# Performance work log

Measured on AMD Instinct MI355X. Metric: run time of the kernel, lower is better.

## Reference

```python
import jax, jax.numpy as jnp
import numpy as np

N, E, B, A = 102400, 1638400, 256, 7


def setup_inputs() -> dict:
    key = jax.random.key(0)
    ks = jax.random.split(key, 24)
    rn = lambda k, s, sc=0.1: jax.random.normal(k, s, jnp.float32) * sc
    return {
        "x": jax.random.normal(ks[0], (N, 5), jnp.float32),
        "edge_index": jax.random.randint(ks[1], (2, E), 0, N, jnp.int32),
        "edge_attr": jax.random.normal(ks[2], (E, 1), jnp.float32),
        "agent_state": jax.random.normal(ks[3], (B, 34), jnp.float32),
        "pool_batch": jnp.sort(jax.random.randint(ks[4], (N,), 0, B, jnp.int32)),
        # GATConv params (heads=1, concat): lin [5,64], lin_edge [1,64], att vectors [64], bias [64]
        "W_gat": rn(ks[5], (5, 64)), "att_src": rn(ks[6], (64,)), "att_dst": rn(ks[7], (64,)),
        "W_edge": rn(ks[8], (1, 64)), "att_edge": rn(ks[9], (64,)), "b_gat": rn(ks[10], (64,)),
        "W_fc1": rn(ks[11], (64, 128)), "b_fc1": rn(ks[12], (128,)),
        "W_fc2": rn(ks[13], (34, 64)), "b_fc2": rn(ks[14], (64,)),
        "W_v1": rn(ks[15], (192, 128)), "b_v1": rn(ks[16], (128,)),
        "W_v2": rn(ks[17], (128, 1)), "b_v2": rn(ks[18], (1,)),
        "W_a1": rn(ks[19], (192, 128)), "b_a1": rn(ks[20], (128,)),
        "W_a2": rn(ks[21], (128, A)), "b_a2": rn(ks[22], (A,)),
    }


def _gat(x, edge_index, edge_attr, W_gat, att_src, att_dst, W_edge, att_edge, b_gat):
    n = x.shape[0]
    # add self-loops (PyG default), self-loop edge_attr = mean of edge_attr
    loop = jnp.arange(n, dtype=edge_index.dtype)
    src = jnp.concatenate([edge_index[0], loop])
    dst = jnp.concatenate([edge_index[1], loop])
    ea = jnp.concatenate([edge_attr, jnp.broadcast_to(edge_attr.mean(0), (n, edge_attr.shape[1]))], 0)
    h = x @ W_gat                                  # [N,64]
    a_s = h @ att_src                              # [N]
    a_d = h @ att_dst                              # [N]
    a_e = (ea @ W_edge) @ att_edge                 # [E+N]
    alpha = jax.nn.leaky_relu(a_s[src] + a_d[dst] + a_e, 0.2)
    # segment softmax over incoming edges per destination node
    m = jax.ops.segment_max(alpha, dst, num_segments=n)
    ex = jnp.exp(alpha - m[dst])
    s = jax.ops.segment_sum(ex, dst, num_segments=n)
    w = ex / (s[dst] + 1e-16)
    out = jax.ops.segment_sum(w[:, None] * h[src], dst, num_segments=n)
    return out + b_gat


def reference(x, edge_index, edge_attr, agent_state, pool_batch,
              W_gat, att_src, att_dst, W_edge, att_edge, b_gat,
              W_fc1, b_fc1, W_fc2, b_fc2,
              W_v1, b_v1, W_v2, b_v2, W_a1, b_a1, W_a2, b_a2):
    h = _gat(x, edge_index, edge_attr, W_gat, att_src, att_dst, W_edge, att_edge, b_gat)
    h = jax.nn.relu(h @ W_fc1 + b_fc1)             # [N,128]
    # global mean pool over graphs
    ssum = jax.ops.segment_sum(h, pool_batch, num_segments=B)
    cnt = jax.ops.segment_sum(jnp.ones((h.shape[0],), h.dtype), pool_batch, num_segments=B)
    g = ssum / jnp.maximum(cnt, 1.0)[:, None]      # [B,128]
    a = jax.nn.relu(agent_state @ W_fc2 + b_fc2)   # [B,64]
    z = jnp.concatenate([g, a], -1)                # [B,192]
    value = jax.nn.relu(z @ W_v1 + b_v1) @ W_v2 + b_v2
    adv = jax.nn.relu(z @ W_a1 + b_a1) @ W_a2 + b_a2
    return value + adv - adv.mean(-1, keepdims=True)
```

## Files before the change

### kernel.cpp

```cpp
#include <hip/hip_runtime.h>
#include <hip/hip_fp16.h>
#include <math.h>

#define NPB   512
#define NPBL  9
#define HSTR  5
#define MAXR  256
#define TILE  2048
#define RPT   8
#define GCS   16
#define EPARTS 256
#define SLICES 8

static __device__ __forceinline__ float lrelu(float x) { return x > 0.0f ? x : 0.2f * x; }

static __device__ __forceinline__ unsigned pk2(float a, float b) {
    __half2 h = __floats2half2_rn(a, b);
    return *reinterpret_cast<unsigned*>(&h);
}


__global__ void k_easum_part(const float* __restrict__ ea, float* __restrict__ part, int n) {
    __shared__ float s[256];
    int t = threadIdx.x;
    int n4 = n >> 2;
    const float4* ea4 = (const float4*)ea;
    float acc = 0.f;
    for (int i = blockIdx.x * 256 + t; i < n4; i += EPARTS * 256) {
        float4 v = ea4[i];
        acc += v.x + v.y + v.z + v.w;
    }
    if (blockIdx.x == 0 && t < (n & 3)) acc += ea[n4 * 4 + t];
    s[t] = acc;
    __syncthreads();
    for (int o = 128; o > 0; o >>= 1) {
        if (t < o) s[t] += s[t + o];
        __syncthreads();
    }
    if (t == 0) part[blockIdx.x] = s[0];
}

__global__ void k_setup(const float* __restrict__ W_gat, const float* __restrict__ att_src,
                        const float* __restrict__ att_dst, const float* __restrict__ W_edge,
                        const float* __restrict__ att_edge, const float* __restrict__ b_gat,
                        const float* __restrict__ W_fc1, const float* __restrict__ b_fc1,
                        const float* __restrict__ part, float* __restrict__ consts) {
    __shared__ float s[128];
    int t = threadIdx.x;
    s[t] = part[t] + part[t + 128];
    __syncthreads();
    for (int o = 64; o > 0; o >>= 1) {
        if (t < o) s[t] += s[t + o];
        __syncthreads();
    }
    if (t == 0) consts[0] = s[0];
    if (t == 0) {
        float c = 0.f;
        for (int k = 0; k < 64; k++) c += W_edge[k] * att_edge[k];
        consts[1] = c;
    }
    if (t < 5) {
        float a = 0.f, b = 0.f;
        for (int c = 0; c < 64; c++) {
            float w = W_gat[t * 64 + c];
            a += w * att_src[c];
            b += w * att_dst[c];
        }
        consts[2 + t] = a;
        consts[7 + t] = b;
    }
    float bcv = b_fc1[t];
    for (int c = 0; c < 64; c++) bcv += b_gat[c] * W_fc1[c * 128 + t];
    consts[16 + t] = bcv;
    for (int k = 0; k < 5; k++) {
        float w = 0.f;
        for (int c = 0; c < 64; c++) w += W_gat[k * 64 + c] * W_fc1[c * 128 + t];
        consts[144 + k * 128 + t] = w;
    }
}

__global__ void k_np1(const float* __restrict__ x, const float* __restrict__ consts,
                      uint4* __restrict__ xh, float* __restrict__ a_s, float* __restrict__ a_d,
                      const int* __restrict__ pb, int* __restrict__ bstart,
                      const int* __restrict__ src, const int* __restrict__ dst,
                      const float* __restrict__ ea,
                      uint2* __restrict__ slab, unsigned* __restrict__ gcur,
                      int N, int B, int E, int R, int CAP, int nbl) {
    if ((int)blockIdx.x < nbl) {
        int i = blockIdx.x * blockDim.x + threadIdx.x;
        if (i >= N) return;
        const float* xi = x + (size_t)i * 5;
        float x0 = xi[0], x1 = xi[1], x2 = xi[2], x3 = xi[3], x4 = xi[4];
        float as = x0 * consts[2] + x1 * consts[3] + x2 * consts[4] + x3 * consts[5] + x4 * consts[6];
        float ad = x0 * consts[7] + x1 * consts[8] + x2 * consts[9] + x3 * consts[10] + x4 * consts[11];
        uint4 pkv;
        pkv.x = pk2(x0, x1);
        pkv.y = pk2(x2, x3);
        pkv.z = pk2(x4, 1.0f);
        pkv.w = __float_as_uint(as);
        xh[i] = pkv;
        a_s[i] = as;
        a_d[i] = ad;
        int cur = pb[i];
        int prev = (i == 0) ? -1 : pb[i - 1];
        for (int b = prev + 1; b <= cur; b++) bstart[b] = i;
        if (i == N - 1)
            for (int b = cur + 1; b <= B; b++) bstart[b] = N;
        return;
    }
    __shared__ unsigned hist[MAXR], lbase[MAXR], gbase[MAXR], scan[256];
    __shared__ uint2 staged[TILE];
    __shared__ unsigned char bof[TILE];
    int t = threadIdx.x;
    int e0 = ((int)blockIdx.x - nbl) * TILE;
    int n = E - e0; if (n > TILE) n = TILE;
    for (int i = t; i < MAXR; i += 256) hist[i] = 0;
    __syncthreads();
    unsigned key[RPT]; float val[RPT]; unsigned brk[RPT];
    float ce = consts[1];
#pragma unroll
    for (int k = 0; k < RPT; k++) {
        int idx = t + k * 256;
        brk[k] = 0xFFFFFFFFu;
        if (idx < n) {
            int e = e0 + idx;
            int d = dst[e];
            unsigned b = (unsigned)d >> NPBL;
            key[k] = ((unsigned)src[e] << NPBL) | ((unsigned)d & (NPB - 1));
            val[k] = ce * ea[e];
            unsigned r = atomicAdd(&hist[b], 1u);
            brk[k] = (b << 12) | r;
        }
    }
    __syncthreads();
    unsigned v = (t < R) ? hist[t] : 0;
    if (t < R) gbase[t] = atomicAdd(&gcur[t * GCS], v);
    scan[t] = v;
    __syncthreads();
    for (int off = 1; off < 256; off <<= 1) {
        unsigned add = (t >= off) ? scan[t - off] : 0;
        __syncthreads();
        scan[t] += add;
        __syncthreads();
    }
    if (t < R) lbase[t] = scan[t] - v;
    __syncthreads();
#pragma unroll
    for (int k = 0; k < RPT; k++) {
        if (brk[k] != 0xFFFFFFFFu) {
            unsigned b = brk[k] >> 12, r = brk[k] & 4095u;
            unsigned pos = lbase[b] + r;
            staged[pos] = make_uint2(key[k], __float_as_uint(val[k]));
            bof[pos] = (unsigned char)b;
        }
    }
    __syncthreads();
    for (int i = t; i < n; i += 256) {
        unsigned b = bof[i];
        unsigned slot = gbase[b] + (unsigned)i - lbase[b];
        if (slot < (unsigned)CAP) slab[(size_t)b * CAP + slot] = staged[i];
    }
}

__global__ void k_p2(const uint2* __restrict__ slab, const unsigned* __restrict__ gcur,
                     const uint4* __restrict__ xh, const float* __restrict__ a_d,
                     float* __restrict__ partials, int S, int CAP, int N) {
    __shared__ __half2 accH[NPB * HSTR];
    __shared__ float adl[NPB];
    int t = threadIdx.x;
    int s = blockIdx.x, r = blockIdx.y;
    for (int i = t; i < NPB; i += 256) {
        int node = r * NPB + i;
        adl[i] = (node < N) ? a_d[node] : 0.f;
    }
    __half2 z2 = __floats2half2_rn(0.f, 0.f);
    for (int i = t; i < NPB * HSTR; i += 256) accH[i] = z2;
    __syncthreads();
    unsigned cnt = gcur[r * GCS]; if (cnt > (unsigned)CAP) cnt = CAP;
    unsigned L = (cnt + (unsigned)S - 1) / (unsigned)S;
    unsigned i0 = (unsigned)s * L, i1 = i0 + L; if (i1 > cnt) i1 = cnt;
    const uint2* sl = slab + (size_t)r * CAP;
    for (unsigned i = i0 + t; i < i1; i += 256) {
        uint2 rec = sl[i];
        uint4 v = xh[rec.x >> NPBL];
        unsigned dl = rec.x & (NPB - 1);
        float al = __uint_as_float(v.w) + adl[dl] + __uint_as_float(rec.y);
        float ex = __expf(lrelu(al));
        __half2 ex2 = __half2half2(__float2half(ex));
        __half2* a = accH + dl * HSTR;
        unsafeAtomicAdd(a + 0, __hmul2(ex2, *reinterpret_cast<const __half2*>(&v.x)));
        unsafeAtomicAdd(a + 1, __hmul2(ex2, *reinterpret_cast<const __half2*>(&v.y)));
        unsafeAtomicAdd(a + 2, __hmul2(ex2, *reinterpret_cast<const __half2*>(&v.z)));
    }
    __syncthreads();
    float* out = partials + (size_t)(r * S + s) * (NPB * 6);
    for (int j = t; j < NPB * 6; j += 256) {
        int comp = j >> NPBL, dl = j & (NPB - 1);
        __half2 h = accH[dl * HSTR + (comp >> 1)];
        out[j] = (comp & 1) ? __high2float(h) : __low2float(h);
    }
}

__global__ void k_p3(const float* __restrict__ partials, const float* __restrict__ x,
                     const float* __restrict__ a_s, const float* __restrict__ a_d,
                     const float* __restrict__ consts, float* __restrict__ y,
                     int N, int S, float inv_E) {
    int i = blockIdx.x * blockDim.x + threadIdx.x;
    if (i >= N) return;
    int r = i >> NPBL, dl = i & (NPB - 1);
    float y0 = 0, y1 = 0, y2 = 0, y3 = 0, y4 = 0, ss = 0;
    const float* p = partials + (size_t)r * S * (NPB * 6) + dl;
    for (int s = 0; s < S; s++) {
        const float* q = p + (size_t)s * (NPB * 6);
        y0 += q[0 * NPB]; y1 += q[1 * NPB]; y2 += q[2 * NPB];
        y3 += q[3 * NPB]; y4 += q[4 * NPB]; ss += q[5 * NPB];
    }
    const float* xi = x + (size_t)i * 5;
    float x0 = xi[0], x1 = xi[1], x2 = xi[2], x3 = xi[3], x4 = xi[4];
    float mean_ea = consts[0] * inv_E;
    float aself = lrelu(a_s[i] + a_d[i] + consts[1] * mean_ea);
    float exs = __expf(aself);
    float inv = 1.f / (ss + exs + 1e-16f);
    y[0 * (size_t)N + i] = (y0 + exs * x0) * inv;
    y[1 * (size_t)N + i] = (y1 + exs * x1) * inv;
    y[2 * (size_t)N + i] = (y2 + exs * x2) * inv;
    y[3 * (size_t)N + i] = (y3 + exs * x3) * inv;
    y[4 * (size_t)N + i] = (y4 + exs * x4) * inv;
}

__global__ void k_pool(const float* __restrict__ y, const float* __restrict__ consts,
                       const int* __restrict__ bstart, float* __restrict__ g4, int B, int N) {
    int l = threadIdx.x;
    int b = blockIdx.x >> 2, q = blockIdx.x & 3;
    int st = bstart[b], en = bstart[b + 1];
    int len = en - st;
    int qlen = (len + 3) >> 2;
    int i0 = st + q * qlen;
    int i1 = i0 + qlen;
    if (i0 > en) i0 = en;
    if (i1 > en) i1 = en;
    float w0 = consts[144 + l], w1 = consts[272 + l], w2 = consts[400 + l],
          w3 = consts[528 + l], w4 = consts[656 + l];
    float bc = consts[16 + l];
    const float* y0 = y;
    const float* y1p = y + (size_t)N;
    const float* y2p = y + 2 * (size_t)N;
    const float* y3p = y + 3 * (size_t)N;
    const float* y4p = y + 4 * (size_t)N;
    float a0 = 0.f, a1 = 0.f, a2 = 0.f, a3 = 0.f;
    int i = i0;
    for (; i + 3 < i1; i += 4) {
        float h0 = bc + y0[i] * w0 + y1p[i] * w1 + y2p[i] * w2 + y3p[i] * w3 + y4p[i] * w4;
        float h1 = bc + y0[i+1] * w0 + y1p[i+1] * w1 + y2p[i+1] * w2 + y3p[i+1] * w3 + y4p[i+1] * w4;
        float h2 = bc + y0[i+2] * w0 + y1p[i+2] * w1 + y2p[i+2] * w2 + y3p[i+2] * w3 + y4p[i+2] * w4;
        float h3 = bc + y0[i+3] * w0 + y1p[i+3] * w1 + y2p[i+3] * w2 + y3p[i+3] * w3 + y4p[i+3] * w4;
        a0 += fmaxf(h0, 0.f);
        a1 += fmaxf(h1, 0.f);
        a2 += fmaxf(h2, 0.f);
        a3 += fmaxf(h3, 0.f);
    }
    for (; i < i1; ++i) {
        float h = bc + y0[i] * w0 + y1p[i] * w1 + y2p[i] * w2 + y3p[i] * w3 + y4p[i] * w4;
        a0 += fmaxf(h, 0.f);
    }
    g4[((size_t)q * B + b) * 128 + l] = (a0 + a1) + (a2 + a3);
}

__global__ void k_head(const float* __restrict__ g4, const int* __restrict__ bstart,
                       const float* __restrict__ agent_state, const float* __restrict__ W_fc2,
                       const float* __restrict__ b_fc2, const float* __restrict__ W_v1,
                       const float* __restrict__ b_v1, const float* __restrict__ W_v2,
                       const float* __restrict__ b_v2, const float* __restrict__ W_a1,
                       const float* __restrict__ b_a1, const float* __restrict__ W_a2,
                       const float* __restrict__ b_a2, float* __restrict__ out, int A, int B) {
    __shared__ float z[192];
    __shared__ float v1s[128], a1s[128], red[128];
    __shared__ float advs[8];
    int b = blockIdx.x, t = threadIdx.x;
    float cnt = (float)(bstart[b + 1] - bstart[b]);
    cnt = cnt < 1.f ? 1.f : cnt;
    z[t] = (g4[(size_t)b * 128 + t] + g4[((size_t)B + b) * 128 + t]
          + g4[(2 * (size_t)B + b) * 128 + t] + g4[(3 * (size_t)B + b) * 128 + t]) / cnt;
    if (t < 64) {
        float a = b_fc2[t];
        const float* as_ = agent_state + b * 34;
        for (int k = 0; k < 34; k++) a += as_[k] * W_fc2[k * 64 + t];
        z[128 + t] = fmaxf(a, 0.f);
    }
    __syncthreads();
    float v = b_v1[t], a = b_a1[t];
#pragma unroll 4
    for (int j = 0; j < 192; j++) {
        float zj = z[j];
        v += zj * W_v1[j * 128 + t];
        a += zj * W_a1[j * 128 + t];
    }
    v1s[t] = fmaxf(v, 0.f);
    a1s[t] = fmaxf(a, 0.f);
    __syncthreads();
    red[t] = v1s[t] * W_v2[t];
    __syncthreads();
    for (int o = 64; o > 0; o >>= 1) {
        if (t < o) red[t] += red[t + o];
        __syncthreads();
    }
    float value = red[0] + b_v2[0];
    if (t < A) {
        float ad = b_a2[t];
        for (int j = 0; j < 128; j++) ad += a1s[j] * W_a2[j * A + t];
        advs[t] = ad;
    }
    __syncthreads();
    if (t == 0) {
        float m = 0.f;
        for (int j = 0; j < A; j++) m += advs[j];
        m *= (1.f / (float)A);
        for (int j = 0; j < A; j++) out[b * A + j] = value + advs[j] - m;
    }
}

extern "C" void kernel_launch(void* const* d_in, const int* in_sizes, int n_in,
                              void* d_out, int out_size, void* d_ws, size_t ws_size,
                              hipStream_t stream) {
    const float* x        = (const float*)d_in[0];
    const int* edge_index = (const int*)d_in[1];
    const float* ea       = (const float*)d_in[2];
    const float* agent    = (const float*)d_in[3];
    const int* pool_batch = (const int*)d_in[4];
    const float* W_gat    = (const float*)d_in[5];
    const float* att_src  = (const float*)d_in[6];
    const float* att_dst  = (const float*)d_in[7];
    const float* W_edge   = (const float*)d_in[8];
    const float* att_edge = (const float*)d_in[9];
    const float* b_gat    = (const float*)d_in[10];
    const float* W_fc1    = (const float*)d_in[11];
    const float* b_fc1    = (const float*)d_in[12];
    const float* W_fc2    = (const float*)d_in[13];
    const float* b_fc2    = (const float*)d_in[14];
    const float* W_v1     = (const float*)d_in[15];
    const float* b_v1     = (const float*)d_in[16];
    const float* W_v2     = (const float*)d_in[17];
    const float* b_v2     = (const float*)d_in[18];
    const float* W_a1     = (const float*)d_in[19];
    const float* b_a1     = (const float*)d_in[20];
    const float* W_a2     = (const float*)d_in[21];
    const float* b_a2     = (const float*)d_in[22];

    const int N = in_sizes[0] / 5;
    const int E = in_sizes[2];
    const int B = in_sizes[3] / 34;
    const int A = out_size / B;
    const float inv_E = 1.0f / (float)E;

    const int* src = edge_index;
    const int* dst = edge_index + E;

    const int R = (N + NPB - 1) / NPB;
    int capBase = (E + R - 1) / R;
    const int CAP = capBase + capBase / 16 + 256;

    char* ws = (char*)d_ws;
    size_t off = 0;
    auto take = [&](size_t bytes) {
        size_t o = off;
        off = (off + bytes + 255) & ~(size_t)255;
        return o;
    };
    size_t o_consts = take(4096);
    size_t o_gcur   = take((size_t)MAXR * GCS * 4);
    size_t zero_bytes = off;
    size_t o_epart  = take((size_t)EPARTS * 4);
    size_t o_xh     = take((size_t)N * 16);
    size_t o_as     = take((size_t)N * 4);
    size_t o_ad     = take((size_t)N * 4);
    size_t o_y      = take((size_t)N * 5 * 4);
    size_t o_bstart = take((size_t)(B + 1) * 4);
    size_t o_g4     = take((size_t)4 * B * 128 * 4);
    size_t o_slab   = take((size_t)R * CAP * 8);
    size_t o_part   = off;
    size_t perS = (size_t)R * NPB * 6 * 4;
    int S = SLICES;
    while (S > 1 && o_part + (size_t)S * perS > ws_size) S--;

    float* consts   = (float*)(ws + o_consts);
    unsigned* gcur  = (unsigned*)(ws + o_gcur);
    float* epart    = (float*)(ws + o_epart);
    uint4* xh       = (uint4*)(ws + o_xh);
    float* a_s      = (float*)(ws + o_as);
    float* a_d      = (float*)(ws + o_ad);
    float* y        = (float*)(ws + o_y);
    int* bstart     = (int*)(ws + o_bstart);
    float* g4       = (float*)(ws + o_g4);
    uint2* slab     = (uint2*)(ws + o_slab);
    float* partials = (float*)(ws + o_part);

    (void)hipMemsetAsync(d_ws, 0, zero_bytes, stream);

    k_easum_part<<<EPARTS, 256, 0, stream>>>(ea, epart, E);
    k_setup<<<1, 128, 0, stream>>>(W_gat, att_src, att_dst, W_edge, att_edge, b_gat,
                                   W_fc1, b_fc1, epart, consts);

    int nbl = (N + 255) / 256;
    int ebl = (E + TILE - 1) / TILE;
    k_np1<<<nbl + ebl, 256, 0, stream>>>(x, consts, xh, a_s, a_d, pool_batch, bstart,
                                         src, dst, ea, slab, gcur, N, B, E, R, CAP, nbl);
    dim3 g2grid(S, R);
    k_p2<<<g2grid, 256, 0, stream>>>(slab, gcur, xh, a_d, partials, S, CAP, N);
    k_p3<<<nbl, 256, 0, stream>>>(partials, x, a_s, a_d, consts, y, N, S, inv_E);
    k_pool<<<4 * B, 128, 0, stream>>>(y, consts, bstart, g4, B, N);
    k_head<<<B, 128, 0, stream>>>(g4, bstart, agent, W_fc2, b_fc2, W_v1, b_v1, W_v2, b_v2,
                                  W_a1, b_a1, W_a2, b_a2, (float*)d_out, A, B);
}
```

Before: 128.2 us.

## Fuse edge-attr sum into scatter pass, drop memset, store fp16 partials

Removes the separate edge_attr reduction kernel and the workspace memset. The edge sum is now accumulated inside the edge-bucketing blocks via per-block reductions and atomics into eight slots, and the zeroing moves into the setup kernel. The final sum is written into consts by one thread of the aggregation kernel, which k_p3 reads afterwards. Per-slice partials are stored as packed half2 instead of fp32, halving partial-buffer traffic at some precision cost in the cross-slice sums.

After: 124.2 us. 3.1% less time.

```diff
diff --git a/kernel.cpp b/kernel.cpp
--- a/kernel.cpp
+++ b/kernel.cpp
@@ -9,7 +9,6 @@
 #define TILE  2048
 #define RPT   8
 #define GCS   16
-#define EPARTS 256
 #define SLICES 8
 
 static __device__ __forceinline__ float lrelu(float x) { return x > 0.0f ? x : 0.2f * x; }
@@ -18,42 +17,21 @@
     __half2 h = __floats2half2_rn(a, b);
     return *reinterpret_cast<unsigned*>(&h);
 }
-
-
-__global__ void k_easum_part(const float* __restrict__ ea, float* __restrict__ part, int n) {
-    __shared__ float s[256];
-    int t = threadIdx.x;
-    int n4 = n >> 2;
-    const float4* ea4 = (const float4*)ea;
-    float acc = 0.f;
-    for (int i = blockIdx.x * 256 + t; i < n4; i += EPARTS * 256) {
-        float4 v = ea4[i];
-        acc += v.x + v.y + v.z + v.w;
-    }
-    if (blockIdx.x == 0 && t < (n & 3)) acc += ea[n4 * 4 + t];
-    s[t] = acc;
-    __syncthreads();
-    for (int o = 128; o > 0; o >>= 1) {
-        if (t < o) s[t] += s[t + o];
-        __syncthreads();
-    }
-    if (t == 0) part[blockIdx.x] = s[0];
-}
+static __device__ __forceinline__ float2 up2(unsigned u) {
+    __half2 h = *reinterpret_cast<__half2*>(&u);
+    return __half22float2(h);
+}
+
 
 __global__ void k_setup(const float* __restrict__ W_gat, const float* __restrict__ att_src,
                         const float* __restrict__ att_dst, const float* __restrict__ W_edge,
                         const float* __restrict__ att_edge, const float* __restrict__ b_gat,
                         const float* __restrict__ W_fc1, const float* __restrict__ b_fc1,
-                        const float* __restrict__ part, float* __restrict__ consts) {
-    __shared__ float s[128];
+                        float* __restrict__ consts, unsigned* __restrict__ gcur,
+                        float* __restrict__ epart8) {
     int t = threadIdx.x;
-    s[t] = part[t] + part[t + 128];
-    __syncthreads();
-    for (int o = 64; o > 0; o >>= 1) {
-        if (t < o) s[t] += s[t + o];
-        __syncthreads();
-    }
-    if (t == 0) consts[0] = s[0];
+    for (int i = t; i < MAXR * GCS; i += 128) gcur[i] = 0u;
+    if (t < 8) epart8[t] = 0.f;
     if (t == 0) {
         float c = 0.f;
         for (int k = 0; k < 64; k++) c += W_edge[k] * att_edge[k];
@@ -85,6 +63,7 @@
                       const int* __restrict__ src, const int* __restrict__ dst,
                       const float* __restrict__ ea,
                       uint2* __restrict__ slab, unsigned* __restrict__ gcur,
+                      float* __restrict__ epart8,
                       int N, int B, int E, int R, int CAP, int nbl) {
     if ((int)blockIdx.x < nbl) {
         int i = blockIdx.x * blockDim.x + threadIdx.x;
@@ -111,6 +90,7 @@
     __shared__ unsigned hist[MAXR], lbase[MAXR], gbase[MAXR], scan[256];
     __shared__ uint2 staged[TILE];
     __shared__ unsigned char bof[TILE];
+    __shared__ float esum[256];
     int t = threadIdx.x;
     int e0 = ((int)blockIdx.x - nbl) * TILE;
     int n = E - e0; if (n > TILE) n = TILE;
@@ -118,6 +98,7 @@
     __syncthreads();
     unsigned key[RPT]; float val[RPT]; unsigned brk[RPT];
     float ce = consts[1];
+    float easc = 0.f;
 #pragma unroll
     for (int k = 0; k < RPT; k++) {
         int idx = t + k * 256;
@@ -127,7 +108,9 @@
             int d = dst[e];
             unsigned b = (unsigned)d >> NPBL;
             key[k] = ((unsigned)src[e] << NPBL) | ((unsigned)d & (NPB - 1));
-            val[k] = ce * ea[e];
+            float eav = ea[e];
+            easc += eav;
+            val[k] = ce * eav;
             unsigned r = atomicAdd(&hist[b], 1u);
             brk[k] = (b << 12) | r;
         }
@@ -160,15 +143,28 @@
         unsigned slot = gbase[b] + (unsigned)i - lbase[b];
         if (slot < (unsigned)CAP) slab[(size_t)b * CAP + slot] = staged[i];
     }
+    esum[t] = easc;
+    __syncthreads();
+    for (int o = 128; o > 0; o >>= 1) {
+        if (t < o) esum[t] += esum[t + o];
+        __syncthreads();
+    }
+    if (t == 0) unsafeAtomicAdd(&epart8[blockIdx.x & 7], esum[0]);
 }
 
 __global__ void k_p2(const uint2* __restrict__ slab, const unsigned* __restrict__ gcur,
                      const uint4* __restrict__ xh, const float* __restrict__ a_d,
-                     float* __restrict__ partials, int S, int CAP, int N) {
+                     unsigned* __restrict__ partials, const float* __restrict__ epart8,
+                     float* __restrict__ consts_w, int S, int CAP, int N) {
     __shared__ __half2 accH[NPB * HSTR];
     __shared__ float adl[NPB];
     int t = threadIdx.x;
     int s = blockIdx.x, r = blockIdx.y;
+    if (s == 0 && r == 0 && t == 0) {
+        float se = 0.f;
+        for (int i = 0; i < 8; i++) se += epart8[i];
+        consts_w[0] = se;
+    }
     for (int i = t; i < NPB; i += 256) {
         int node = r * NPB + i;
         adl[i] = (node < N) ? a_d[node] : 0.f;
@@ -193,39 +189,40 @@
         unsafeAtomicAdd(a + 2, __hmul2(ex2, *reinterpret_cast<const __half2*>(&v.z)));
     }
     __syncthreads();
-    float* out = partials + (size_t)(r * S + s) * (NPB * 6);
-    for (int j = t; j < NPB * 6; j += 256) {
+    unsigned* out = partials + (size_t)(r * S + s) * (NPB * 3);
+    for (int j = t; j < NPB * 3; j += 256) {
         int comp = j >> NPBL, dl = j & (NPB - 1);
-        __half2 h = accH[dl * HSTR + (comp >> 1)];
-        out[j] = (comp & 1) ? __high2float(h) : __low2float(h);
-    }
-}
-
-__global__ void k_p3(const float* __restrict__ partials, const float* __restrict__ x,
+        out[j] = *reinterpret_cast<unsigned*>(&accH[dl * HSTR + comp]);
+    }
+}
+
+__global__ void k_p3(const unsigned* __restrict__ partials, const float* __restrict__ x,
                      const float* __restrict__ a_s, const float* __restrict__ a_d,
                      const float* __restrict__ consts, float* __restrict__ y,
                      int N, int S, float inv_E) {
     int i = blockIdx.x * blockDim.x + threadIdx.x;
     if (i >= N) return;
     int r = i >> NPBL, dl = i & (NPB - 1);
-    float y0 = 0, y1 = 0, y2 = 0, y3 = 0, y4 = 0, ss = 0;
-    const float* p = partials + (size_t)r * S * (NPB * 6) + dl;
+    float2 y01 = make_float2(0.f, 0.f), y23 = make_float2(0.f, 0.f), y4s = make_float2(0.f, 0.f);
+    const unsigned* p = partials + (size_t)r * S * (NPB * 3) + dl;
     for (int s = 0; s < S; s++) {
-        const float* q = p + (size_t)s * (NPB * 6);
-        y0 += q[0 * NPB]; y1 += q[1 * NPB]; y2 += q[2 * NPB];
-        y3 += q[3 * NPB]; y4 += q[4 * NPB]; ss += q[5 * NPB];
+        const unsigned* q = p + (size_t)s * (NPB * 3);
+        float2 a = up2(q[0 * NPB]), b = up2(q[1 * NPB]), c = up2(q[2 * NPB]);
+        y01.x += a.x; y01.y += a.y;
+        y23.x += b.x; y23.y += b.y;
+        y4s.x += c.x; y4s.y += c.y;
     }
     const float* xi = x + (size_t)i * 5;
     float x0 = xi[0], x1 = xi[1], x2 = xi[2], x3 = xi[3], x4 = xi[4];
     float mean_ea = consts[0] * inv_E;
     float aself = lrelu(a_s[i] + a_d[i] + consts[1] * mean_ea);
     float exs = __expf(aself);
-    float inv = 1.f / (ss + exs + 1e-16f);
-    y[0 * (size_t)N + i] = (y0 + exs * x0) * inv;
-    y[1 * (size_t)N + i] = (y1 + exs * x1) * inv;
-    y[2 * (size_t)N + i] = (y2 + exs * x2) * inv;
-    y[3 * (size_t)N + i] = (y3 + exs * x3) * inv;
-    y[4 * (size_t)N + i] = (y4 + exs * x4) * inv;
+    float inv = 1.f / (y4s.y + exs + 1e-16f);
+    y[0 * (size_t)N + i] = (y01.x + exs * x0) * inv;
+    y[1 * (size_t)N + i] = (y01.y + exs * x1) * inv;
+    y[2 * (size_t)N + i] = (y23.x + exs * x2) * inv;
+    y[3 * (size_t)N + i] = (y23.y + exs * x3) * inv;
+    y[4 * (size_t)N + i] = (y4s.x + exs * x4) * inv;
 }
 
 __global__ void k_pool(const float* __restrict__ y, const float* __restrict__ consts,
@@ -368,8 +365,7 @@
     };
     size_t o_consts = take(4096);
     size_t o_gcur   = take((size_t)MAXR * GCS * 4);
-    size_t zero_bytes = off;
-    size_t o_epart  = take((size_t)EPARTS * 4);
+    size_t o_epart8 = take(8 * 4);
     size_t o_xh     = take((size_t)N * 16);
     size_t o_as     = take((size_t)N * 4);
     size_t o_ad     = take((size_t)N * 4);
@@ -378,13 +374,13 @@
     size_t o_g4     = take((size_t)4 * B * 128 * 4);
     size_t o_slab   = take((size_t)R * CAP * 8);
     size_t o_part   = off;
-    size_t perS = (size_t)R * NPB * 6 * 4;
+    size_t perS = (size_t)R * NPB * 3 * 4;
     int S = SLICES;
     while (S > 1 && o_part + (size_t)S * perS > ws_size) S--;
 
     float* consts   = (float*)(ws + o_consts);
     unsigned* gcur  = (unsigned*)(ws + o_gcur);
-    float* epart    = (float*)(ws + o_epart);
+    float* epart8   = (float*)(ws + o_epart8);
     uint4* xh       = (uint4*)(ws + o_xh);
     float* a_s      = (float*)(ws + o_as);
     float* a_d      = (float*)(ws + o_ad);
@@ -392,20 +388,18 @@
     int* bstart     = (int*)(ws + o_bstart);
     float* g4       = (float*)(ws + o_g4);
     uint2* slab     = (uint2*)(ws + o_slab);
-    float* partials = (float*)(ws + o_part);
-
-    (void)hipMemsetAsync(d_ws, 0, zero_bytes, stream);
-
-    k_easum_part<<<EPARTS, 256, 0, stream>>>(ea, epart, E);
+    unsigned* partials = (unsigned*)(ws + o_part);
+
     k_setup<<<1, 128, 0, stream>>>(W_gat, att_src, att_dst, W_edge, att_edge, b_gat,
-                                   W_fc1, b_fc1, epart, consts);
+                                   W_fc1, b_fc1, consts, gcur, epart8);
 
     int nbl = (N + 255) / 256;
     int ebl = (E + TILE - 1) / TILE;
     k_np1<<<nbl + ebl, 256, 0, stream>>>(x, consts, xh, a_s, a_d, pool_batch, bstart,
-                                         src, dst, ea, slab, gcur, N, B, E, R, CAP, nbl);
+                                         src, dst, ea, slab, gcur, epart8,
+                                         N, B, E, R, CAP, nbl);
     dim3 g2grid(S, R);
-    k_p2<<<g2grid, 256, 0, stream>>>(slab, gcur, xh, a_d, partials, S, CAP, N);
+    k_p2<<<g2grid, 256, 0, stream>>>(slab, gcur, xh, a_d, partials, epart8, consts, S, CAP, N);
     k_p3<<<nbl, 256, 0, stream>>>(partials, x, a_s, a_d, consts, y, N, S, inv_E);
     k_pool<<<4 * B, 128, 0, stream>>>(y, consts, bstart, g4, B, N);
     k_head<<<B, 128, 0, stream>>>(g4, bstart, agent, W_fc2, b_fc2, W_v1, b_v1, W_v2, b_v2,
```
